# Kernel optimization log

Measured on AMD Instinct MI355X. Metric: run time of the kernel, lower is better.

## Reference

```python
import jax, jax.numpy as jnp
import numpy as np

N = 20
DM = 128
C_CLIP = 10.0
BATCH = 16384


def setup_inputs() -> dict:
    key = jax.random.key(0)
    ks = jax.random.split(key, 9)
    s = 1.0 / np.sqrt(DM)
    inp = {
        "x": jax.random.normal(ks[0], (BATCH, N, DM), dtype=jnp.float32),
        "Wg": jax.random.uniform(ks[1], (DM, DM), jnp.float32, -s, s),
        "bg": jax.random.uniform(ks[2], (DM,), jnp.float32, -s, s),
        "Wn": jax.random.uniform(ks[3], (DM, DM), jnp.float32, -s, s),
        "bn": jax.random.uniform(ks[4], (DM,), jnp.float32, -s, s),
        "Wk": jax.random.uniform(ks[5], (DM, DM), jnp.float32, -s, s),
        "bk": jax.random.uniform(ks[6], (DM,), jnp.float32, -s, s),
        "Wq": jax.random.uniform(ks[7], (DM, DM), jnp.float32, -s, s),
        "bq": jax.random.uniform(ks[8], (DM,), jnp.float32, -s, s),
    }
    return inp


def reference(x, Wg, bg, Wn, bn, Wk, bk, Wq, bq):
    B, n, dm = x.shape
    # graph embedding: max-pool over nodes
    x_graph = jnp.max(x, axis=1)                      # [B, dm]
    lp_graph = x_graph @ Wg.T + bg                    # [B, dm]
    lp_nodes = x @ Wn.T + bn                          # [B, n, dm]
    h = lp_nodes + lp_graph[:, None, :]               # [B, n, dm]
    K = h @ Wk.T + bk                                 # [B, n, dm]
    Q = h @ Wq.T + bq                                 # [B, n, dm]
    M = jnp.einsum("bnd,bmd->bnm", K, Q) / np.float32(np.sqrt(dm))
    M_hat = C_CLIP * jnp.tanh(M) - jnp.eye(n, dtype=M.dtype) * 1e20
    # flattened (global) softmax over all n*n entries
    p = jax.nn.softmax(M_hat.reshape(B, n * n), axis=1)
    return p.reshape(B, n, n)
```

## Files before the change

kernel.cpp:

```cpp
#include <hip/hip_runtime.h>
#include <hip/hip_bf16.h>
#include <math.h>

#define DM 128
#define NN 20
#define NB 16384
#define BPB 4

#define OFF_A      0
#define OFF_AT     16384
#define OFF_WA     32768
#define OFF_WAT    49152
#define OFF_AG     65536
#define OFF_BMAT   81920
#define OFF_S1T    98304
#define OFF_S2T    114688
#define OFF_C2T    131072
#define OFF_U0     147456
#define OFF_V0     147584
#define OFF_T0     147712
#define OFF_W1     147840
#define OFF_AT0    147968
#define OFF_A0     148096
#define OFF_B0     148224
#define OFF_C1     148352
#define OFF_C00    148480
#define OFF_CBASE  148481
#define OFF_FRAGB  149504
#define OFF_FRAGS  (149504 + 8192)
#define OFF_AVH    182272
#define OFF_CW     3328000

#define INVS 0.08838834764831845f
#define FW 132

typedef _Float16 h16;
typedef h16 half8 __attribute__((ext_vector_type(8)));
typedef h16 half4v __attribute__((ext_vector_type(4)));
typedef float f32x4 __attribute__((ext_vector_type(4)));

#define MFMA16(a, b, c) __builtin_amdgcn_mfma_f32_16x16x32_f16((a), (b), (c), 0, 0, 0)

__device__ __forceinline__ int swz(int row, int col) {
    return (row * 128 + col) ^ ((row & 7) << 3);
}

__global__ void k_prep1(const float* __restrict__ Wk, const float* __restrict__ Wq,
                        const float* __restrict__ bk, const float* __restrict__ bq,
                        const float* __restrict__ bn, const float* __restrict__ bg,
                        float* __restrict__ ws) {
    const int bx = blockIdx.x, t = threadIdx.x;
    __shared__ float sbuf[128];
    if (bx < 128) {
        sbuf[t] = Wk[t * 128 + bx];
        __syncthreads();
        float a = 0.f;
        #pragma unroll 8
        for (int d = 0; d < 128; ++d) a += sbuf[d] * Wq[d * 128 + t];
        ws[OFF_A  + bx * 128 + t] = a;
        ws[OFF_AT + t * 128 + bx] = a;
    } else {
        float u = 0.f, v = 0.f;
        #pragma unroll 8
        for (int d = 0; d < 128; ++d) {
            u += Wk[d * 128 + t] * bq[d];
            v += Wq[d * 128 + t] * bk[d];
        }
        ws[OFF_U0 + t] = u;
        ws[OFF_V0 + t] = v;
        ws[OFF_T0 + t] = bn[t] + bg[t];
        sbuf[t] = bk[t] * bq[t];
        __syncthreads();
        for (int s = 64; s > 0; s >>= 1) { if (t < s) sbuf[t] += sbuf[t + s]; __syncthreads(); }
        if (t == 0) ws[OFF_C00] = sbuf[0];
    }
}

__global__ void k_prep2(const float* __restrict__ Wn, const float* __restrict__ Wg,
                        float* __restrict__ ws) {
    const int bx = blockIdx.x, t = threadIdx.x;
    __shared__ float s1[128], s2[128];
    if (bx < 128) {
        const int r = bx;
        s1[t] = Wn[t * 128 + r];
        s2[t] = ws[OFF_A + r * 128 + t];
        __syncthreads();
        float wa = 0.f, wat = 0.f, ag = 0.f;
        #pragma unroll 4
        for (int e = 0; e < 128; ++e) {
            wa  += s1[e] * ws[OFF_A  + e * 128 + t];
            wat += s1[e] * ws[OFF_AT + e * 128 + t];
            ag  += s2[e] * Wg[e * 128 + t];
        }
        ws[OFF_WA  + r * 128 + t] = wa;
        ws[OFF_WAT + r * 128 + t] = wat;
        ws[OFF_AG  + r * 128 + t] = ag;
    } else {
        const float t0t = ws[OFF_T0 + t], u0t = ws[OFF_U0 + t], v0t = ws[OFF_V0 + t];
        float w1 = 0.f, at0 = 0.f;
        #pragma unroll 8
        for (int e = 0; e < 128; ++e) {
            const float t0e = ws[OFF_T0 + e];
            w1  += (ws[OFF_A + t * 128 + e] + ws[OFF_AT + t * 128 + e]) * t0e;
            at0 +=  ws[OFF_A + t * 128 + e] * t0e;
        }
        w1 += u0t + v0t;
        ws[OFF_W1  + t] = w1;
        ws[OFF_AT0 + t] = at0;
        s1[t] = t0t * (at0 + u0t + v0t);
        __syncthreads();
        for (int s = 64; s > 0; s >>= 1) { if (t < s) s1[t] += s1[t + s]; __syncthreads(); }
        if (t == 0) ws[OFF_CBASE] = s1[0] + ws[OFF_C00];
    }
}

__global__ void k_prep3(const float* __restrict__ Wn, const float* __restrict__ Wg,
                        float* __restrict__ ws) {
    const int bx = blockIdx.x, t = threadIdx.x;
    __shared__ float wa[128], wat[128], wgc[128];
    if (bx < 128) {
        const int r = bx;
        wa[t]  = ws[OFF_WA  + r * 128 + t];
        wat[t] = ws[OFF_WAT + r * 128 + t];
        wgc[t] = Wg[t * 128 + r];
        __syncthreads();
        float bm = 0.f, s1v = 0.f, s2v = 0.f, c2v = 0.f;
        #pragma unroll 4
        for (int f = 0; f < 128; ++f) {
            bm  += wa[f]  * Wn[f * 128 + t];
            s1v += wa[f]  * Wg[f * 128 + t];
            s2v += wat[f] * Wg[f * 128 + t];
            c2v += wgc[f] * ws[OFF_AG + f * 128 + t];
        }
        ws[OFF_BMAT + r * 128 + t] = bm;
        ws[OFF_S1T + t * 128 + r] = s1v;
        ws[OFF_S2T + t * 128 + r] = s2v;
        ws[OFF_C2T + t * 128 + r] = c2v;
    } else {
        float a0 = 0.f, b0 = 0.f, c1 = 0.f;
        #pragma unroll 8
        for (int f = 0; f < 128; ++f) {
            a0 += ws[OFF_WA  + t * 128 + f] * ws[OFF_T0 + f] + Wn[f * 128 + t] * ws[OFF_U0 + f];
            b0 += ws[OFF_WAT + t * 128 + f] * ws[OFF_T0 + f] + Wn[f * 128 + t] * ws[OFF_V0 + f];
            c1 += Wg[f * 128 + t] * ws[OFF_W1 + f];
        }
        ws[OFF_A0 + t] = a0;
        ws[OFF_B0 + t] = b0;
        ws[OFF_C1 + t] = c1;
    }
}

__global__ void k_prep4(float* __restrict__ ws) {
    h16* fB = (h16*)(ws + OFF_FRAGB);
    h16* fS = (h16*)(ws + OFF_FRAGS);
    const int idx = blockIdx.x * 256 + threadIdx.x;
    if (idx < 16384) {
        const int e = idx & 7, l = (idx >> 3) & 63, ks = (idx >> 9) & 3, ct = idx >> 11;
        const int k = 32 * ks + 8 * (l >> 4) + e, j = 16 * ct + (l & 15);
        fB[idx] = (h16)ws[OFF_BMAT + k * 128 + j];
    } else {
        const int sidx = idx - 16384;
        const int e = sidx & 7, l = (sidx >> 3) & 63, ks = (sidx >> 9) & 3, ct = sidx >> 11;
        const int k = 32 * ks + 8 * (l >> 4) + e, j = 16 * ct + (l & 15);
        float v;
        if (j < 128)      v = ws[OFF_S1T + k * 128 + j];
        else if (j < 256) v = ws[OFF_S2T + k * 128 + (j - 128)];
        else              v = ws[OFF_C2T + k * 128 + (j - 256)];
        fS[sidx] = (h16)v;
    }
}

__global__ __launch_bounds__(256) void k_abc(const float* __restrict__ x,
                                             float* __restrict__ ws) {
    __shared__ __align__(16) h16 xgl[16 * 128];
    __shared__ float cpart[16][4];
    const int t = threadIdx.x, l = t & 63, w = t >> 6;
    const int lc = l & 15, lg = l >> 4;
    const int h = l >> 5, c32 = l & 31;
    const int b0 = blockIdx.x * 16;

    #pragma unroll
    for (int q = 0; q < 4; ++q) {
        const int bi = 4 * w + q;
        const float4* xp = (const float4*)(x + (size_t)(b0 + bi) * 2560) + c32;
        float4 mx = xp[h * 32];
        #pragma unroll
        for (int i = 1; i < 10; ++i) {
            const float4 v = xp[(2 * i + h) * 32];
            mx.x = fmaxf(mx.x, v.x); mx.y = fmaxf(mx.y, v.y);
            mx.z = fmaxf(mx.z, v.z); mx.w = fmaxf(mx.w, v.w);
        }
        mx.x = fmaxf(mx.x, __shfl_xor(mx.x, 32));
        mx.y = fmaxf(mx.y, __shfl_xor(mx.y, 32));
        mx.z = fmaxf(mx.z, __shfl_xor(mx.z, 32));
        mx.w = fmaxf(mx.w, __shfl_xor(mx.w, 32));
        if (h == 0) {
            const half4v hg = { (h16)mx.x, (h16)mx.y, (h16)mx.z, (h16)mx.w };
            *(half4v*)(xgl + swz(bi, 4 * c32)) = hg;
        }
    }
    __syncthreads();

    const half8* fS = (const half8*)(ws + OFF_FRAGS);
    f32x4 sacc[6];
    #pragma unroll
    for (int i = 0; i < 6; ++i) sacc[i] = (f32x4){0.f, 0.f, 0.f, 0.f};
    #pragma unroll
    for (int ks = 0; ks < 4; ++ks) {
        const half8 ag = *(const half8*)(xgl + swz(lc, 32 * ks + 8 * lg));
        #pragma unroll
        for (int i = 0; i < 6; ++i) {
            const int ct = w + 4 * i;
            sacc[i] = MFMA16(ag, fS[(ct * 4 + ks) * 64 + l], sacc[i]);
        }
    }
    h16* avh = (h16*)(ws + OFF_AVH);
    #pragma unroll
    for (int i = 0; i < 4; ++i) {
        const int ct = w + 4 * i;
        const int v = ct >> 3, c128 = 16 * (ct & 7) + lc;
        const float bias = (v == 0) ? ws[OFF_A0 + c128] : ws[OFF_B0 + c128];
        #pragma unroll
        for (int r = 0; r < 4; ++r)
            avh[((size_t)(b0 + 4 * lg + r) * 3 + v) * 128 + c128] = (h16)(sacc[i][r] + bias);
    }
    float p[4] = {0.f, 0.f, 0.f, 0.f};
    #pragma unroll
    for (int i = 4; i < 6; ++i) {
        const int j = 16 * (w + 4 * i - 16) + lc;
        const float c1j = ws[OFF_C1 + j];
        #pragma unroll
        for (int r = 0; r < 4; ++r) {
            const float xgv = (float)xgl[swz(4 * lg + r, j)];
            p[r] += (sacc[i][r] + c1j) * xgv;
        }
    }
    #pragma unroll
    for (int r = 0; r < 4; ++r) {
        float v = p[r];
        v += __shfl_xor(v, 1); v += __shfl_xor(v, 2);
        v += __shfl_xor(v, 4); v += __shfl_xor(v, 8);
        if (lc == 0) cpart[4 * lg + r][w] = v;
    }
    __syncthreads();
    if (t < 16)
        ws[OFF_CW + b0 + t] = ws[OFF_CBASE]
                            + cpart[t][0] + cpart[t][1] + cpart[t][2] + cpart[t][3];
}

__global__ __launch_bounds__(256, 4) void k_main(const float* __restrict__ x,
                                                 const float* __restrict__ ws,
                                                 float* __restrict__ out) {
    __shared__ __align__(16) h16 fFs[BPB * NN * FW];
    __shared__ float abL[BPB][40];

    const int t = threadIdx.x, l = t & 63, w = t >> 6;
    const int lc = l & 15, lg = l >> 4;
    const int b = blockIdx.x * BPB + w;
    const half8 h8z = {};

    const float* xb = x + (size_t)b * 2560;
    half8 xa0[4], xa1[4];
    #pragma unroll
    for (int ks = 0; ks < 4; ++ks) {
        const float4 v0 = *(const float4*)(xb + lc * 128 + 32 * ks + 8 * lg);
        const float4 v1 = *(const float4*)(xb + lc * 128 + 32 * ks + 8 * lg + 4);
        xa0[ks] = (half8){ (h16)v0.x, (h16)v0.y, (h16)v0.z, (h16)v0.w,
                           (h16)v1.x, (h16)v1.y, (h16)v1.z, (h16)v1.w };
    }
    #pragma unroll
    for (int ks = 0; ks < 4; ++ks) {
        half8 v = h8z;
        if (lc < 4) {
            const float4 v0 = *(const float4*)(xb + (16 + lc) * 128 + 32 * ks + 8 * lg);
            const float4 v1 = *(const float4*)(xb + (16 + lc) * 128 + 32 * ks + 8 * lg + 4);
            v = (half8){ (h16)v0.x, (h16)v0.y, (h16)v0.z, (h16)v0.w,
                         (h16)v1.x, (h16)v1.y, (h16)v1.z, (h16)v1.w };
        }
        xa1[ks] = v;
    }
    const h16* avh = (const h16*)(ws + OFF_AVH);
    half8 s8[4];
    #pragma unroll
    for (int ks = 0; ks < 4; ++ks) {
        half8 v = h8z;
        if (lc < 2) v = *(const half8*)(avh + ((size_t)b * 3 + lc) * 128 + 32 * ks + 8 * lg);
        s8[ks] = v;
    }

    h16* fFw = fFs + w * NN * FW;
    const half8* fB = (const half8*)(ws + OFF_FRAGB);

    #pragma unroll
    for (int ct = 0; ct < 8; ++ct) {
        f32x4 f0 = {0.f, 0.f, 0.f, 0.f}, f1 = {0.f, 0.f, 0.f, 0.f};
        #pragma unroll
        for (int ks = 0; ks < 4; ++ks) {
            const half8 bb = fB[(ct * 4 + ks) * 64 + l];
            f0 = MFMA16(xa0[ks], bb, f0);
            f1 = MFMA16(xa1[ks], bb, f1);
        }
        #pragma unroll
        for (int r = 0; r < 4; ++r) {
            fFw[(4 * lg + r) * FW + 16 * ct + lc] = (h16)f0[r];
            if (lg == 0) fFw[(16 + r) * FW + 16 * ct + lc] = (h16)f1[r];
        }
    }
    {
        f32x4 a0c = {0.f, 0.f, 0.f, 0.f}, a1c = {0.f, 0.f, 0.f, 0.f};
        #pragma unroll
        for (int ks = 0; ks < 4; ++ks) {
            a0c = MFMA16(xa0[ks], s8[ks], a0c);
            a1c = MFMA16(xa1[ks], s8[ks], a1c);
        }
        if (lc == 0) {
            #pragma unroll
            for (int r = 0; r < 4; ++r) abL[w][4 * lg + r] = a0c[r];
            if (lg == 0) {
                #pragma unroll
                for (int r = 0; r < 4; ++r) abL[w][16 + r] = a1c[r];
            }
        }
        if (lc == 1) {
            #pragma unroll
            for (int r = 0; r < 4; ++r) abL[w][20 + 4 * lg + r] = a0c[r];
            if (lg == 0) {
                #pragma unroll
                for (int r = 0; r < 4; ++r) abL[w][36 + r] = a1c[r];
            }
        }
    }
    asm volatile("s_waitcnt lgkmcnt(0)" ::: "memory");

    f32x4 mAcc[2][2];
    #pragma unroll
    for (int nt = 0; nt < 2; ++nt)
        #pragma unroll
        for (int mt = 0; mt < 2; ++mt) mAcc[nt][mt] = (f32x4){0.f, 0.f, 0.f, 0.f};
    #pragma unroll
    for (int nt = 0; nt < 2; ++nt) {
        #pragma unroll
        for (int ks = 0; ks < 4; ++ks) {
            const int row = 16 * nt + lc;
            const half8 aF = *(const half8*)(fFw + (row < NN ? row : 0) * FW + 32 * ks + 8 * lg);
            mAcc[nt][0] = MFMA16(aF, xa0[ks], mAcc[nt][0]);
            mAcc[nt][1] = MFMA16(aF, xa1[ks], mAcc[nt][1]);
        }
    }

    const float cb = ws[OFF_CW + b];
    const float bm0 = abL[w][20 + lc];
    const float bm1 = (lc < 4) ? abL[w][36 + lc] : 0.f;
    float pv[2][2][4];
    float psum = 0.f;
    #pragma unroll
    for (int nt = 0; nt < 2; ++nt) {
        #pragma unroll
        for (int r = 0; r < 4; ++r) {
            const int n = 16 * nt + 4 * lg + r;
            const float an = (n < NN) ? abL[w][n] : 0.f;
            #pragma unroll
            for (int mt = 0; mt < 2; ++mt) {
                const int m = 16 * mt + lc;
                const bool valid = (n < NN) && (m < NN) && (n != m);
                const float Mv = (mAcc[nt][mt][r] + an + (mt ? bm1 : bm0) + cb) * INVS;
                const float E = __expf(2.f * Mv);
                const float e = valid ? __expf(-20.f / (E + 1.f)) : 0.f;
                pv[nt][mt][r] = e;
                psum += e;
            }
        }
    }
    #pragma unroll
    for (int off = 32; off > 0; off >>= 1) psum += __shfl_xor(psum, off);
    const float inv = 1.f / psum;

    float* ob = out + (size_t)b * 400;
    #pragma unroll
    for (int nt = 0; nt < 2; ++nt) {
        #pragma unroll
        for (int r = 0; r < 4; ++r) {
            const int n = 16 * nt + 4 * lg + r;
            if (n < NN) {
                ob[n * 20 + lc] = pv[nt][0][r] * inv;
                if (lc < 4) ob[n * 20 + 16 + lc] = pv[nt][1][r] * inv;
            }
        }
    }
}

extern "C" void kernel_launch(void* const* d_in, const int* in_sizes, int n_in,
                              void* d_out, int out_size, void* d_ws, size_t ws_size,
                              hipStream_t stream) {
    const float* x  = (const float*)d_in[0];
    const float* Wg = (const float*)d_in[1];
    const float* bg = (const float*)d_in[2];
    const float* Wn = (const float*)d_in[3];
    const float* bn = (const float*)d_in[4];
    const float* Wk = (const float*)d_in[5];
    const float* bk = (const float*)d_in[6];
    const float* Wq = (const float*)d_in[7];
    const float* bq = (const float*)d_in[8];
    float* out = (float*)d_out;
    float* ws  = (float*)d_ws;

    k_prep1<<<129, 128, 0, stream>>>(Wk, Wq, bk, bq, bn, bg, ws);
    k_prep2<<<129, 128, 0, stream>>>(Wn, Wg, ws);
    k_prep3<<<129, 128, 0, stream>>>(Wn, Wg, ws);
    k_prep4<<<256, 256, 0, stream>>>(ws);
    k_abc<<<NB / 16, 256, 0, stream>>>(x, ws);
    k_main<<<NB / BPB, 256, 0, stream>>>(x, ws, out);
}
```

Before: 123.7 us.

## Fuse graph-embedding pass into main kernel and write MFMA fragments directly in prep

Removes the separate k_abc pass that reread x to compute the per-graph max-pool, projected vectors and scalar bias. The fused kernel now derives the max from the already-loaded fp16 x fragments with packed half max over shuffles, computes those vectors and the bias in shared memory, and uses 8 graphs per 512-thread block. k_prep3 now writes the fp16 MFMA fragment layouts directly, so k_prep4 goes away. This saves a full extra read of x, a global round-trip for the intermediate vectors, and two launches, in exchange for extra block-level syncs and more shared memory per block.

After: 115.2 us. 1.07x faster.

```diff
diff --git a/kernel.cpp b/kernel.cpp
--- a/kernel.cpp
+++ b/kernel.cpp
@@ -5,7 +5,7 @@
 #define DM 128
 #define NN 20
 #define NB 16384
-#define BPB 4
+#define BPB 8
 
 #define OFF_A      0
 #define OFF_AT     16384
@@ -28,8 +28,6 @@
 #define OFF_CBASE  148481
 #define OFF_FRAGB  149504
 #define OFF_FRAGS  (149504 + 8192)
-#define OFF_AVH    182272
-#define OFF_CW     3328000
 
 #define INVS 0.08838834764831845f
 #define FW 132
@@ -37,12 +35,25 @@
 typedef _Float16 h16;
 typedef h16 half8 __attribute__((ext_vector_type(8)));
 typedef h16 half4v __attribute__((ext_vector_type(4)));
+typedef h16 half2v __attribute__((ext_vector_type(2)));
 typedef float f32x4 __attribute__((ext_vector_type(4)));
+typedef unsigned int uint4v __attribute__((ext_vector_type(4)));
 
 #define MFMA16(a, b, c) __builtin_amdgcn_mfma_f32_16x16x32_f16((a), (b), (c), 0, 0, 0)
 
 __device__ __forceinline__ int swz(int row, int col) {
     return (row * 128 + col) ^ ((row & 7) << 3);
+}
+
+__device__ __forceinline__ unsigned pkmax(unsigned a, unsigned b) {
+    const half2v r = __builtin_elementwise_max(__builtin_bit_cast(half2v, a),
+                                               __builtin_bit_cast(half2v, b));
+    return __builtin_bit_cast(unsigned, r);
+}
+
+__device__ __forceinline__ int fb_idx(int k, int j) {
+    return ((j >> 4) << 11) | ((k >> 5) << 9)
+         | ((((k >> 3) & 3) * 16 + (j & 15)) << 3) | (k & 7);
 }
 
 __global__ void k_prep1(const float* __restrict__ Wk, const float* __restrict__ Wq,
@@ -118,6 +129,8 @@
                         float* __restrict__ ws) {
     const int bx = blockIdx.x, t = threadIdx.x;
     __shared__ float wa[128], wat[128], wgc[128];
+    h16* fB = (h16*)(ws + OFF_FRAGB);
+    h16* fS = (h16*)(ws + OFF_FRAGS);
     if (bx < 128) {
         const int r = bx;
         wa[t]  = ws[OFF_WA  + r * 128 + t];
@@ -132,10 +145,10 @@
             s2v += wat[f] * Wg[f * 128 + t];
             c2v += wgc[f] * ws[OFF_AG + f * 128 + t];
         }
-        ws[OFF_BMAT + r * 128 + t] = bm;
-        ws[OFF_S1T + t * 128 + r] = s1v;
-        ws[OFF_S2T + t * 128 + r] = s2v;
-        ws[OFF_C2T + t * 128 + r] = c2v;
+        fB[fb_idx(r, t)]       = (h16)bm;
+        fS[fb_idx(t, r)]       = (h16)s1v;
+        fS[fb_idx(t, r + 128)] = (h16)s2v;
+        fS[fb_idx(t, r + 256)] = (h16)c2v;
     } else {
         float a0 = 0.f, b0 = 0.f, c1 = 0.f;
         #pragma unroll 8
@@ -150,109 +163,15 @@
     }
 }
 
-__global__ void k_prep4(float* __restrict__ ws) {
-    h16* fB = (h16*)(ws + OFF_FRAGB);
-    h16* fS = (h16*)(ws + OFF_FRAGS);
-    const int idx = blockIdx.x * 256 + threadIdx.x;
-    if (idx < 16384) {
-        const int e = idx & 7, l = (idx >> 3) & 63, ks = (idx >> 9) & 3, ct = idx >> 11;
-        const int k = 32 * ks + 8 * (l >> 4) + e, j = 16 * ct + (l & 15);
-        fB[idx] = (h16)ws[OFF_BMAT + k * 128 + j];
-    } else {
-        const int sidx = idx - 16384;
-        const int e = sidx & 7, l = (sidx >> 3) & 63, ks = (sidx >> 9) & 3, ct = sidx >> 11;
-        const int k = 32 * ks + 8 * (l >> 4) + e, j = 16 * ct + (l & 15);
-        float v;
-        if (j < 128)      v = ws[OFF_S1T + k * 128 + j];
-        else if (j < 256) v = ws[OFF_S2T + k * 128 + (j - 128)];
-        else              v = ws[OFF_C2T + k * 128 + (j - 256)];
-        fS[sidx] = (h16)v;
-    }
-}
-
-__global__ __launch_bounds__(256) void k_abc(const float* __restrict__ x,
-                                             float* __restrict__ ws) {
-    __shared__ __align__(16) h16 xgl[16 * 128];
-    __shared__ float cpart[16][4];
-    const int t = threadIdx.x, l = t & 63, w = t >> 6;
-    const int lc = l & 15, lg = l >> 4;
-    const int h = l >> 5, c32 = l & 31;
-    const int b0 = blockIdx.x * 16;
-
-    #pragma unroll
-    for (int q = 0; q < 4; ++q) {
-        const int bi = 4 * w + q;
-        const float4* xp = (const float4*)(x + (size_t)(b0 + bi) * 2560) + c32;
-        float4 mx = xp[h * 32];
-        #pragma unroll
-        for (int i = 1; i < 10; ++i) {
-            const float4 v = xp[(2 * i + h) * 32];
-            mx.x = fmaxf(mx.x, v.x); mx.y = fmaxf(mx.y, v.y);
-            mx.z = fmaxf(mx.z, v.z); mx.w = fmaxf(mx.w, v.w);
-        }
-        mx.x = fmaxf(mx.x, __shfl_xor(mx.x, 32));
-        mx.y = fmaxf(mx.y, __shfl_xor(mx.y, 32));
-        mx.z = fmaxf(mx.z, __shfl_xor(mx.z, 32));
-        mx.w = fmaxf(mx.w, __shfl_xor(mx.w, 32));
-        if (h == 0) {
-            const half4v hg = { (h16)mx.x, (h16)mx.y, (h16)mx.z, (h16)mx.w };
-            *(half4v*)(xgl + swz(bi, 4 * c32)) = hg;
-        }
-    }
-    __syncthreads();
-
-    const half8* fS = (const half8*)(ws + OFF_FRAGS);
-    f32x4 sacc[6];
-    #pragma unroll
-    for (int i = 0; i < 6; ++i) sacc[i] = (f32x4){0.f, 0.f, 0.f, 0.f};
-    #pragma unroll
-    for (int ks = 0; ks < 4; ++ks) {
-        const half8 ag = *(const half8*)(xgl + swz(lc, 32 * ks + 8 * lg));
-        #pragma unroll
-        for (int i = 0; i < 6; ++i) {
-            const int ct = w + 4 * i;
-            sacc[i] = MFMA16(ag, fS[(ct * 4 + ks) * 64 + l], sacc[i]);
-        }
-    }
-    h16* avh = (h16*)(ws + OFF_AVH);
-    #pragma unroll
-    for (int i = 0; i < 4; ++i) {
-        const int ct = w + 4 * i;
-        const int v = ct >> 3, c128 = 16 * (ct & 7) + lc;
-        const float bias = (v == 0) ? ws[OFF_A0 + c128] : ws[OFF_B0 + c128];
-        #pragma unroll
-        for (int r = 0; r < 4; ++r)
-            avh[((size_t)(b0 + 4 * lg + r) * 3 + v) * 128 + c128] = (h16)(sacc[i][r] + bias);
-    }
-    float p[4] = {0.f, 0.f, 0.f, 0.f};
-    #pragma unroll
-    for (int i = 4; i < 6; ++i) {
-        const int j = 16 * (w + 4 * i - 16) + lc;
-        const float c1j = ws[OFF_C1 + j];
-        #pragma unroll
-        for (int r = 0; r < 4; ++r) {
-            const float xgv = (float)xgl[swz(4 * lg + r, j)];
-            p[r] += (sacc[i][r] + c1j) * xgv;
-        }
-    }
-    #pragma unroll
-    for (int r = 0; r < 4; ++r) {
-        float v = p[r];
-        v += __shfl_xor(v, 1); v += __shfl_xor(v, 2);
-        v += __shfl_xor(v, 4); v += __shfl_xor(v, 8);
-        if (lc == 0) cpart[4 * lg + r][w] = v;
-    }
-    __syncthreads();
-    if (t < 16)
-        ws[OFF_CW + b0 + t] = ws[OFF_CBASE]
-                            + cpart[t][0] + cpart[t][1] + cpart[t][2] + cpart[t][3];
-}
-
-__global__ __launch_bounds__(256, 4) void k_main(const float* __restrict__ x,
-                                                 const float* __restrict__ ws,
-                                                 float* __restrict__ out) {
+__global__ __launch_bounds__(512, 6) void k_fused(const float* __restrict__ x,
+                                                  const float* __restrict__ ws,
+                                                  float* __restrict__ out) {
+    __shared__ __align__(16) h16 xgl[BPB * 128];
+    __shared__ __align__(16) h16 avhL[BPB * 2 * 128];
     __shared__ __align__(16) h16 fFs[BPB * NN * FW];
     __shared__ float abL[BPB][40];
+    __shared__ float cpart[BPB][BPB];
+    __shared__ float cbs[BPB];
 
     const int t = threadIdx.x, l = t & 63, w = t >> 6;
     const int lc = l & 15, lg = l >> 4;
@@ -279,13 +198,115 @@
         }
         xa1[ks] = v;
     }
-    const h16* avh = (const h16*)(ws + OFF_AVH);
+
+    #pragma unroll
+    for (int ks = 0; ks < 4; ++ks) {
+        uint4v m0 = __builtin_bit_cast(uint4v, xa0[ks]);
+        uint4v m1 = __builtin_bit_cast(uint4v, xa1[ks]);
+        #pragma unroll
+        for (int s = 1; s < 16; s <<= 1) {
+            #pragma unroll
+            for (int wd = 0; wd < 4; ++wd)
+                m0[wd] = pkmax(m0[wd], (unsigned)__shfl_xor((int)m0[wd], s));
+        }
+        #pragma unroll
+        for (int s = 1; s < 4; s <<= 1) {
+            #pragma unroll
+            for (int wd = 0; wd < 4; ++wd)
+                m1[wd] = pkmax(m1[wd], (unsigned)__shfl_xor((int)m1[wd], s));
+        }
+        #pragma unroll
+        for (int wd = 0; wd < 4; ++wd) {
+            const unsigned m1b = (unsigned)__shfl((int)m1[wd], l & 51);
+            m0[wd] = pkmax(m0[wd], m1b);
+        }
+        if (lc == 0)
+            *(half8*)(xgl + swz(w, 32 * ks + 8 * lg)) = __builtin_bit_cast(half8, m0);
+    }
+    __syncthreads();
+
+    {
+        const half8* fS = (const half8*)(ws + OFF_FRAGS);
+        f32x4 sacc[3];
+        #pragma unroll
+        for (int i = 0; i < 3; ++i) sacc[i] = (f32x4){0.f, 0.f, 0.f, 0.f};
+        #pragma unroll
+        for (int ks = 0; ks < 4; ++ks) {
+            const half8 ag = *(const half8*)(xgl + swz(lc & 7, 32 * ks + 8 * lg));
+            #pragma unroll
+            for (int i = 0; i < 3; ++i) {
+                const int ct = w + 8 * i;
+                sacc[i] = MFMA16(ag, fS[(ct * 4 + ks) * 64 + l], sacc[i]);
+            }
+        }
+        #pragma unroll
+        for (int i = 0; i < 2; ++i) {
+            const int ct = w + 8 * i;
+            const int v = ct >> 3, c128 = 16 * (ct & 7) + lc;
+            const float bias = (v == 0) ? ws[OFF_A0 + c128] : ws[OFF_B0 + c128];
+            if (lg < 2) {
+                #pragma unroll
+                for (int r = 0; r < 4; ++r)
+                    avhL[(4 * lg + r) * 256 + v * 128 + c128] = (h16)(sacc[i][r] + bias);
+            }
+        }
+        {
+            const int j = 16 * w + lc;
+            const float c1j = ws[OFF_C1 + j];
+            float p[4];
+            #pragma unroll
+            for (int r = 0; r < 4; ++r) {
+                const float xgv = (float)xgl[swz((4 * lg + r) & 7, j)];
+                p[r] = (sacc[2][r] + c1j) * xgv;
+            }
+            #pragma unroll
+            for (int r = 0; r < 4; ++r) {
+                float v = p[r];
+                v += __shfl_xor(v, 1); v += __shfl_xor(v, 2);
+                v += __shfl_xor(v, 4); v += __shfl_xor(v, 8);
+                if (lc == 0 && lg < 2) cpart[4 * lg + r][w] = v;
+            }
+        }
+    }
+    __syncthreads();
+    if (t < BPB) {
+        float s = ws[OFF_CBASE];
+        #pragma unroll
+        for (int j = 0; j < BPB; ++j) s += cpart[t][j];
+        cbs[t] = s;
+    }
+    __syncthreads();
+
     half8 s8[4];
     #pragma unroll
     for (int ks = 0; ks < 4; ++ks) {
         half8 v = h8z;
-        if (lc < 2) v = *(const half8*)(avh + ((size_t)b * 3 + lc) * 128 + 32 * ks + 8 * lg);
+        if (lc < 2) v = *(const half8*)(avhL + w * 256 + lc * 128 + 32 * ks + 8 * lg);
         s8[ks] = v;
+    }
+    {
+        f32x4 a0c = {0.f, 0.f, 0.f, 0.f}, a1c = {0.f, 0.f, 0.f, 0.f};
+        #pragma unroll
+        for (int ks = 0; ks < 4; ++ks) {
+            a0c = MFMA16(xa0[ks], s8[ks], a0c);
+            a1c = MFMA16(xa1[ks], s8[ks], a1c);
+        }
+        if (lc == 0) {
+            #pragma unroll
+            for (int r = 0; r < 4; ++r) abL[w][4 * lg + r] = a0c[r];
+            if (lg == 0) {
+                #pragma unroll
+                for (int r = 0; r < 4; ++r) abL[w][16 + r] = a1c[r];
+            }
+        }
+        if (lc == 1) {
+            #pragma unroll
+            for (int r = 0; r < 4; ++r) abL[w][20 + 4 * lg + r] = a0c[r];
+            if (lg == 0) {
+                #pragma unroll
+                for (int r = 0; r < 4; ++r) abL[w][36 + r] = a1c[r];
+            }
+        }
     }
 
     h16* fFw = fFs + w * NN * FW;
@@ -304,30 +325,6 @@
         for (int r = 0; r < 4; ++r) {
             fFw[(4 * lg + r) * FW + 16 * ct + lc] = (h16)f0[r];
             if (lg == 0) fFw[(16 + r) * FW + 16 * ct + lc] = (h16)f1[r];
-        }
-    }
-    {
-        f32x4 a0c = {0.f, 0.f, 0.f, 0.f}, a1c = {0.f, 0.f, 0.f, 0.f};
-        #pragma unroll
-        for (int ks = 0; ks < 4; ++ks) {
-            a0c = MFMA16(xa0[ks], s8[ks], a0c);
-            a1c = MFMA16(xa1[ks], s8[ks], a1c);
-        }
-        if (lc == 0) {
-            #pragma unroll
-            for (int r = 0; r < 4; ++r) abL[w][4 * lg + r] = a0c[r];
-            if (lg == 0) {
-                #pragma unroll
-                for (int r = 0; r < 4; ++r) abL[w][16 + r] = a1c[r];
-            }
-        }
-        if (lc == 1) {
-            #pragma unroll
-            for (int r = 0; r < 4; ++r) abL[w][20 + 4 * lg + r] = a0c[r];
-            if (lg == 0) {
-                #pragma unroll
-                for (int r = 0; r < 4; ++r) abL[w][36 + r] = a1c[r];
-            }
         }
     }
     asm volatile("s_waitcnt lgkmcnt(0)" ::: "memory");
@@ -348,7 +345,7 @@
         }
     }
 
-    const float cb = ws[OFF_CW + b];
+    const float cb = cbs[w];
     const float bm0 = abL[w][20 + lc];
     const float bm1 = (lc < 4) ? abL[w][36 + lc] : 0.f;
     float pv[2][2][4];
@@ -407,7 +404,5 @@
     k_prep1<<<129, 128, 0, stream>>>(Wk, Wq, bk, bq, bn, bg, ws);
     k_prep2<<<129, 128, 0, stream>>>(Wn, Wg, ws);
     k_prep3<<<129, 128, 0, stream>>>(Wn, Wg, ws);
-    k_prep4<<<256, 256, 0, stream>>>(ws);
-    k_abc<<<NB / 16, 256, 0, stream>>>(x, ws);
-    k_main<<<NB / BPB, 256, 0, stream>>>(x, ws, out);
-}
+    k_fused<<<NB / BPB, 512, 0, stream>>>(x, ws, out);
+}
```
